# Optimization experiments

Measured on AMD Instinct MI355X. Metric: run time of the kernel, lower is better.

Reference implementation:

```python
import jax, jax.numpy as jnp
import numpy as np

N, E, G = 50000, 800000, 200
F_IN, C, HEADS = 16, 64, 4
HID = C * HEADS  # 256


def setup_inputs() -> dict:
    key = jax.random.key(0)
    ks = jax.random.split(key, 30)
    rn = lambda k, s, sc=0.1: jax.random.normal(k, s, jnp.float32) * sc
    inp = {
        'x': jax.random.normal(ks[0], (N, F_IN), jnp.float32),
        'edge_index': jax.random.randint(ks[1], (2, E), 0, N, jnp.int32),
        'batch': jnp.sort(jax.random.randint(ks[2], (N,), 0, G, jnp.int32)),
        'Wl1': rn(ks[3], (F_IN, HID)), 'Wr1': rn(ks[4], (F_IN, HID)),
        'att1': rn(ks[5], (HEADS, C)), 'b1': rn(ks[6], (HID,)),
        'g1': jnp.ones((HID,), jnp.float32), 'be1': jnp.zeros((HID,), jnp.float32),
        'Wl2': rn(ks[7], (HID, HID)), 'Wr2': rn(ks[8], (HID, HID)),
        'att2': rn(ks[9], (HEADS, C)), 'b2': rn(ks[10], (HID,)),
        'g2': jnp.ones((HID,), jnp.float32), 'be2': jnp.zeros((HID,), jnp.float32),
        # GATv2 layer 3: 256 -> 64, 1 head, mean (concat=False)
        'Wl3': rn(ks[11], (HID, C)), 'Wr3': rn(ks[12], (HID, C)),
        'att3': rn(ks[13], (1, C)), 'b3': rn(ks[14], (C,)),
        'g3': jnp.ones((C,), jnp.float32), 'be3': jnp.zeros((C,), jnp.float32),
        # classifier MLP: 128 -> 64 -> 1
        'Wc1': rn(ks[15], (2 * C, C)), 'bc1': rn(ks[16], (C,)),
        'Wc2': rn(ks[17], (C, 1)), 'bc2': rn(ks[18], (1,)),
    }
    return inp


def _gatv2(x, src, dst, Wl, Wr, att, b, heads, c, concat):
    n = x.shape[0]
    xl = (x @ Wl).reshape(n, heads, c)
    xr = (x @ Wr).reshape(n, heads, c)
    s = jax.nn.leaky_relu(xl[src] + xr[dst], 0.2)       # [E', H, C]
    e = jnp.einsum('ehc,hc->eh', s, att)                 # [E', H]
    m = jax.ops.segment_max(e, dst, num_segments=n)
    p = jnp.exp(e - m[dst])
    denom = jax.ops.segment_sum(p, dst, num_segments=n)
    alpha = p / (denom[dst] + 1e-16)
    out = jax.ops.segment_sum(alpha[:, :, None] * xl[src], dst, num_segments=n)
    out = out.reshape(n, heads * c) if concat else out.mean(axis=1)
    return out + b


def _bn(x, g, b):
    mu = x.mean(0)
    v = x.var(0)
    return (x - mu) * jax.lax.rsqrt(v + 1e-5) * g + b


def reference(x, edge_index, batch,
              Wl1, Wr1, att1, b1, g1, be1,
              Wl2, Wr2, att2, b2, g2, be2,
              Wl3, Wr3, att3, b3, g3, be3,
              Wc1, bc1, Wc2, bc2):
    n = x.shape[0]
    loop = jnp.arange(n, dtype=edge_index.dtype)
    src = jnp.concatenate([edge_index[0], loop])  # PyG add_self_loops=True
    dst = jnp.concatenate([edge_index[1], loop])

    h = _gatv2(x, src, dst, Wl1, Wr1, att1, b1, HEADS, C, True)
    h = jax.nn.elu(_bn(h, g1, be1))  # dropout disabled (eval)
    h = _gatv2(h, src, dst, Wl2, Wr2, att2, b2, HEADS, C, True)
    h = jax.nn.elu(_bn(h, g2, be2))
    h = _gatv2(h, src, dst, Wl3, Wr3, att3, b3, 1, C, False)
    h = _bn(h, g3, be3)

    cnt = jax.ops.segment_sum(jnp.ones((n, 1), h.dtype), batch, num_segments=G)
    mean_pool = jax.ops.segment_sum(h, batch, num_segments=G) / jnp.maximum(cnt, 1.0)
    max_pool = jax.ops.segment_max(h, batch, num_segments=G)
    pooled = jnp.concatenate([mean_pool, max_pool], axis=1)  # [G, 128]

    out = jax.nn.relu(pooled @ Wc1 + bc1)
    out = out @ Wc2 + bc2  # [G, 1]
    return out
```

## Files before the change

kernel.cpp:

```cpp
#include <hip/hip_runtime.h>
#include <math.h>

#define N_NODES 50000
#define N_EDGES 800000
#define ET (N_EDGES + N_NODES)
#define N_GRAPHS 200
#define F_INN 16
#define C_DIM 64
#define N_HEADS 4
#define HIDD 256
#define SCAN_BLOCKS ((N_NODES + 255) / 256)

typedef __attribute__((ext_vector_type(8))) short short8;
typedef __attribute__((ext_vector_type(8))) ushort ushort8;
typedef __attribute__((ext_vector_type(4))) float f32x4;
typedef __attribute__((ext_vector_type(2))) float f32x2;
typedef __attribute__((ext_vector_type(2))) _Float16 h16x2;

#define LOG2E 1.44269504088896340736f

__device__ __forceinline__ float ex2(float x) {
#if __has_builtin(__builtin_amdgcn_exp2f)
  return __builtin_amdgcn_exp2f(x);
#else
  return exp2f(x);
#endif
}

__device__ __forceinline__ h16x2 bc16(unsigned u) {
  union { unsigned u; h16x2 h; } c; c.u = u; return c.h;
}
__device__ __forceinline__ ushort f2h(float f) {
  union { _Float16 h; ushort u; } c; c.h = (_Float16)f; return c.u;
}

#if __has_builtin(__builtin_amdgcn_cvt_pkrtz)
using hw2 = decltype(__builtin_amdgcn_cvt_pkrtz(0.f, 0.f));
__device__ __forceinline__ h16x2 pkrtz(float a, float b) {
  union { hw2 w; h16x2 h; } c;
  c.w = __builtin_amdgcn_cvt_pkrtz(a, b);
  return c.h;
}
#else
__device__ __forceinline__ h16x2 pkrtz(float a, float b) {
  h16x2 r; r[0] = (_Float16)a; r[1] = (_Float16)b; return r;
}
#endif

__device__ __forceinline__ float fdot2f(h16x2 a, h16x2 b, float c) {
#if __has_builtin(__builtin_amdgcn_fdot2) && __has_builtin(__builtin_amdgcn_cvt_pkrtz)
  union { h16x2 h; hw2 w; } ca, cb;
  ca.h = a; cb.h = b;
  return __builtin_amdgcn_fdot2(ca.w, cb.w, c, false);
#else
  return (float)a[0] * (float)b[0] + (float)a[1] * (float)b[1] + c;
#endif
}
__device__ __forceinline__ h16x2 hmax2(h16x2 a, h16x2 b) {
#if __has_builtin(__builtin_elementwise_max)
  return __builtin_elementwise_max(a, b);
#else
  h16x2 r; r[0] = a[0] > b[0] ? a[0] : b[0]; r[1] = a[1] > b[1] ? a[1] : b[1]; return r;
#endif
}
__device__ __forceinline__ unsigned permu(unsigned s0, unsigned s1, unsigned sel) {
#if __has_builtin(__builtin_amdgcn_perm)
  return __builtin_amdgcn_perm(s0, s1, sel);
#else
  unsigned long long cat = (((unsigned long long)s0) << 32) | s1;
  unsigned r = 0;
  for (int i = 0; i < 4; ++i) {
    unsigned b = (sel >> (8 * i)) & 0xff;
    r |= ((unsigned)((cat >> (8 * (b & 7))) & 0xff)) << (8 * i);
  }
  return r;
#endif
}
#define PAIR_LO(A, B) permu((B), (A), 0x05040100u)
#define PAIR_HI(A, B) permu((B), (A), 0x07060302u)

template<int K, int M>
__global__ __launch_bounds__(256) void gemm_dual(
    const float* __restrict__ A, const float* __restrict__ Bl,
    const float* __restrict__ Br, ushort* __restrict__ Clb,
    ushort* __restrict__ Crb, int nrows)
{
  __shared__ __align__(16) float As[16][64];
  __shared__ __align__(16) float Bls[16][64];
  __shared__ __align__(16) float Brs[16][64];
  int tid = threadIdx.x;
  int row0 = blockIdx.x * 64;
  int col0 = blockIdx.y * 64;
  int tr = (tid >> 4) << 2;
  int tc = (tid & 15) << 2;
  float accL[4][4] = {{0.f}}, accR[4][4] = {{0.f}};
  int arow = tid >> 2, ak = (tid & 3) << 2;
  int brow = tid >> 4, bcol = (tid & 15) << 2;
  for (int k0 = 0; k0 < K; k0 += 16) {
    float4 av = make_float4(0.f, 0.f, 0.f, 0.f);
    int gr = row0 + arow;
    if (gr < nrows) av = *(const float4*)&A[(size_t)gr * K + k0 + ak];
    As[ak + 0][arow] = av.x;
    As[ak + 1][arow] = av.y;
    As[ak + 2][arow] = av.z;
    As[ak + 3][arow] = av.w;
    *(float4*)&Bls[brow][bcol] = *(const float4*)&Bl[(size_t)(k0 + brow) * M + col0 + bcol];
    *(float4*)&Brs[brow][bcol] = *(const float4*)&Br[(size_t)(k0 + brow) * M + col0 + bcol];
    __syncthreads();
    #pragma unroll
    for (int k = 0; k < 16; ++k) {
      float4 a = *(const float4*)&As[k][tr];
      float4 bl = *(const float4*)&Bls[k][tc];
      float4 br = *(const float4*)&Brs[k][tc];
      float aa[4] = {a.x, a.y, a.z, a.w};
      float lb[4] = {bl.x, bl.y, bl.z, bl.w};
      float rb[4] = {br.x, br.y, br.z, br.w};
      #pragma unroll
      for (int ii = 0; ii < 4; ++ii)
        #pragma unroll
        for (int jj = 0; jj < 4; ++jj) {
          accL[ii][jj] = fmaf(aa[ii], lb[jj], accL[ii][jj]);
          accR[ii][jj] = fmaf(aa[ii], rb[jj], accR[ii][jj]);
        }
    }
    __syncthreads();
  }
  #pragma unroll
  for (int ii = 0; ii < 4; ++ii) {
    int gr = row0 + tr + ii;
    if (gr < nrows) {
      *(ushort4*)&Clb[(size_t)gr * M + col0 + tc] =
          make_ushort4(f2h(accL[ii][0]), f2h(accL[ii][1]),
                       f2h(accL[ii][2]), f2h(accL[ii][3]));
      *(ushort4*)&Crb[(size_t)gr * M + col0 + tc] =
          make_ushort4(f2h(accR[ii][0]), f2h(accR[ii][1]),
                       f2h(accR[ii][2]), f2h(accR[ii][3]));
    }
  }
}

__device__ __forceinline__ void split_bf16(float a, ushort& hi, ushort& lo) {
  unsigned u = __float_as_uint(a);
  hi = (ushort)(u >> 16);
  float ah = __uint_as_float(u & 0xffff0000u);
  float r = a - ah;
  lo = (ushort)(__float_as_uint(r) >> 16);
}

template<int K, int N>
__global__ void convertB(const float* __restrict__ W, ushort* __restrict__ BTmat) {
  int idx = blockIdx.x * blockDim.x + threadIdx.x;
  if (idx >= K * N) return;
  int k = idx / N, n = idx - k * N;
  ushort hi, lo;
  split_bf16(W[idx], hi, lo);
  size_t dst = ((size_t)(k >> 3) * N + n) * 8 + (k & 7);
  BTmat[dst] = hi;
  BTmat[(size_t)(K / 8) * N * 8 + dst] = lo;
}

template<int N>
__global__ __launch_bounds__(N * 2) void gemm_fused(
    const float* __restrict__ H, const float* __restrict__ gsum,
    const float* __restrict__ gsumsq, const float* __restrict__ g,
    const float* __restrict__ be, const ushort* __restrict__ BT,
    ushort* __restrict__ Clb, ushort* __restrict__ Crb)
{
  constexpr int THREADS = N * 2;
  constexpr int PLANE = 32 * N * 8;
  __shared__ float SCs[256], SHs[256];
  __shared__ ushort Ah_s[32 * 256];
  __shared__ ushort Al_s[32 * 256];
  const int tid = threadIdx.x;
  const int brow0 = blockIdx.x * 32;

  const float invn = 1.0f / (float)N_NODES;
  for (int c = tid; c < 256; c += THREADS) {
    float mu = gsum[c] * invn;
    float var = gsumsq[c] * invn - mu * mu;
    float sc = g[c] * rsqrtf(var + 1e-5f);
    SCs[c] = sc;
    SHs[c] = be[c] - mu * sc;
  }
  __syncthreads();

  for (int gid = tid; gid < 1024; gid += THREADS) {
    int r = gid >> 5;
    int ch0 = (gid & 31) * 8;
    int grow = min(brow0 + r, N_NODES - 1);
    float4 v0 = *(const float4*)&H[(size_t)grow * 256 + ch0];
    float4 v1 = *(const float4*)&H[(size_t)grow * 256 + ch0 + 4];
    float4 sc0 = *(const float4*)&SCs[ch0];
    float4 sc1 = *(const float4*)&SCs[ch0 + 4];
    float4 sh0 = *(const float4*)&SHs[ch0];
    float4 sh1 = *(const float4*)&SHs[ch0 + 4];
    float vv[8] = {v0.x, v0.y, v0.z, v0.w, v1.x, v1.y, v1.z, v1.w};
    float scv[8] = {sc0.x, sc0.y, sc0.z, sc0.w, sc1.x, sc1.y, sc1.z, sc1.w};
    float shv[8] = {sh0.x, sh0.y, sh0.z, sh0.w, sh1.x, sh1.y, sh1.z, sh1.w};
    short8 hi8, lo8;
    #pragma unroll
    for (int j = 0; j < 8; ++j) {
      float t = fmaf(vv[j], scv[j], shv[j]);
      float e = t > 0.f ? t : __expf(t) - 1.f;
      ushort h, l;
      split_bf16(e, h, l);
      hi8[j] = (short)h;
      lo8[j] = (short)l;
    }
    int off = r * 512 + ((ch0 * 2) ^ ((r & 7) << 4));
    *(short8*)((char*)Ah_s + off) = hi8;
    *(short8*)((char*)Al_s + off) = lo8;
  }
  __syncthreads();

  const int wave = tid >> 6, lane = tid & 63;
  const int cn = lane & 15, kgrp = lane >> 4;
  const int combc = wave * 64;
  const bool isR = combc >= N;
  const ushort* Bh = BT + (isR ? 2 * PLANE : 0);
  const ushort* Bl_ = Bh + PLANE;
  const int cb = combc & (N - 1);
  f32x4 acc[2][4];
  #pragma unroll
  for (int rt = 0; rt < 2; ++rt)
    #pragma unroll
    for (int ct = 0; ct < 4; ++ct) acc[rt][ct] = (f32x4)(0.f);

  #pragma unroll 2
  for (int k0 = 0; k0 < 256; k0 += 32) {
    short8 ah[2], al[2];
    #pragma unroll
    for (int rt = 0; rt < 2; ++rt) {
      int row = rt * 16 + cn;
      int off = row * 512 + (((k0 * 2) + kgrp * 16) ^ ((row & 7) << 4));
      ah[rt] = *(const short8*)((const char*)Ah_s + off);
      al[rt] = *(const short8*)((const char*)Al_s + off);
    }
    const size_t bbase = (size_t)((k0 >> 3) + kgrp) * (N * 8);
    #pragma unroll
    for (int ct = 0; ct < 4; ++ct) {
      const size_t bo = bbase + (size_t)(cb + ct * 16 + cn) * 8;
      short8 bh = *(const short8*)&Bh[bo];
      short8 bl = *(const short8*)&Bl_[bo];
      #pragma unroll
      for (int rt = 0; rt < 2; ++rt) {
        acc[rt][ct] = __builtin_amdgcn_mfma_f32_16x16x32_bf16(ah[rt], bh, acc[rt][ct], 0, 0, 0);
        acc[rt][ct] = __builtin_amdgcn_mfma_f32_16x16x32_bf16(ah[rt], bl, acc[rt][ct], 0, 0, 0);
        acc[rt][ct] = __builtin_amdgcn_mfma_f32_16x16x32_bf16(al[rt], bh, acc[rt][ct], 0, 0, 0);
      }
    }
  }

  #pragma unroll
  for (int ct = 0; ct < 4; ++ct) {
    int cc = cb + ct * 16 + cn;
    #pragma unroll
    for (int rt = 0; rt < 2; ++rt) {
      int crow0 = brow0 + rt * 16 + kgrp * 4;
      #pragma unroll
      for (int j = 0; j < 4; ++j) {
        int rr = crow0 + j;
        if (rr < N_NODES) {
          if (!isR) Clb[(size_t)rr * N + cc] = f2h(acc[rt][ct][j]);
          else      Crb[(size_t)rr * N + cc] = f2h(acc[rt][ct][j]);
        }
      }
    }
  }
}

__global__ void hist_kernel(const int* __restrict__ dsts, int* __restrict__ curs) {
  int i = blockIdx.x * blockDim.x + threadIdx.x;
  if (i >= ET) return;
  int d = (i < N_EDGES) ? dsts[i] : i - N_EDGES;
  atomicAdd(&curs[d], 1);
}

__global__ __launch_bounds__(256) void scan_part(
    const int* __restrict__ curs, int* __restrict__ rows, int* __restrict__ bsum)
{
  __shared__ int tmp[256];
  int t = threadIdx.x;
  int i = blockIdx.x * 256 + t;
  int v = (i < N_NODES) ? curs[i] : 0;
  tmp[t] = v;
  __syncthreads();
  #pragma unroll
  for (int off = 1; off < 256; off <<= 1) {
    int u = (t >= off) ? tmp[t - off] : 0;
    __syncthreads();
    tmp[t] += u;
    __syncthreads();
  }
  if (i < N_NODES) rows[i] = tmp[t] - v;
  if (t == 255) bsum[blockIdx.x] = tmp[255];
}

__global__ __launch_bounds__(256) void scan_bsums(
    const int* __restrict__ bsum, int* __restrict__ boff)
{
  __shared__ int tmp[256];
  int t = threadIdx.x;
  int v = (t < SCAN_BLOCKS) ? bsum[t] : 0;
  tmp[t] = v;
  __syncthreads();
  #pragma unroll
  for (int off = 1; off < 256; off <<= 1) {
    int u = (t >= off) ? tmp[t - off] : 0;
    __syncthreads();
    tmp[t] += u;
    __syncthreads();
  }
  if (t < SCAN_BLOCKS) boff[t] = tmp[t] - v;
}

__global__ __launch_bounds__(256) void scan_apply(
    int* __restrict__ rows, const int* __restrict__ boff, int* __restrict__ curs)
{
  int i = blockIdx.x * 256 + threadIdx.x;
  if (i < N_NODES) {
    int r = rows[i] + boff[blockIdx.x];
    rows[i] = r;
    curs[i] = r;
  }
  if (i == 0) rows[N_NODES] = ET;
}

__global__ void scatter_kernel(const int* __restrict__ srcs, const int* __restrict__ dsts,
                               int* __restrict__ curs, int* __restrict__ esrc) {
  int i = blockIdx.x * blockDim.x + threadIdx.x;
  if (i >= ET) return;
  int s, d;
  if (i < N_EDGES) { s = srcs[i]; d = dsts[i]; } else { s = d = i - N_EDGES; }
  int pos = atomicAdd(&curs[d], 1);
  esrc[pos] = s;
}

__global__ __launch_bounds__(256) void flash256(
    const ushort* __restrict__ xl, const ushort* __restrict__ xr,
    const float* __restrict__ att, const int* __restrict__ rows,
    const int* __restrict__ esrc, float* __restrict__ out)
{
  const int wave = threadIdx.x >> 6, lane = threadIdx.x & 63;
  const int d = blockIdx.x * 4 + wave;
  const unsigned lo4 = lane * 4;
  int beg = rows[d], end = rows[d + 1];
  uint2 urx = *(const uint2*)&xr[(size_t)d * 256 + lo4];
  h16x2 x01 = bc16(urx.x), x23 = bc16(urx.y);
  float4 w = *(const float4*)&att[lo4];
  h16x2 w01 = pkrtz(w.x * LOG2E, w.y * LOG2E);
  h16x2 w23 = pkrtz(w.z * LOG2E, w.w * LOG2E);
  const _Float16 c2 = (_Float16)0.2f;
  const h16x2 c02 = {c2, c2};
  auto score = [&](uint2 u) -> float {
    h16x2 v01 = bc16(u.x) + x01;
    h16x2 v23 = bc16(u.y) + x23;
    v01 = hmax2(v01, v01 * c02);
    v23 = hmax2(v23, v23 * c02);
    return fdot2f(v01, w01, fdot2f(v23, w23, 0.f));
  };
  float m = -INFINITY, s = 0.f;
  float a0 = 0.f, a1 = 0.f, a2 = 0.f, a3 = 0.f;
  int p = beg;
  for (; p + 4 <= end; p += 4) {
    int s1 = esrc[p], s2 = esrc[p + 1], s3 = esrc[p + 2], s4 = esrc[p + 3];
    uint2 u1 = *(const uint2*)&xl[((unsigned)s1 << 8) + lo4];
    uint2 u2 = *(const uint2*)&xl[((unsigned)s2 << 8) + lo4];
    uint2 u3 = *(const uint2*)&xl[((unsigned)s3 << 8) + lo4];
    uint2 u4 = *(const uint2*)&xl[((unsigned)s4 << 8) + lo4];
    float e1 = score(u1);
    float e2 = score(u2);
    float e3 = score(u3);
    float e4 = score(u4);
    e1 += __shfl_xor(e1, 1); e2 += __shfl_xor(e2, 1);
    e3 += __shfl_xor(e3, 1); e4 += __shfl_xor(e4, 1);
    e1 += __shfl_xor(e1, 2); e2 += __shfl_xor(e2, 2);
    e3 += __shfl_xor(e3, 2); e4 += __shfl_xor(e4, 2);
    e1 += __shfl_xor(e1, 4); e2 += __shfl_xor(e2, 4);
    e3 += __shfl_xor(e3, 4); e4 += __shfl_xor(e4, 4);
    e1 += __shfl_xor(e1, 8); e2 += __shfl_xor(e2, 8);
    e3 += __shfl_xor(e3, 8); e4 += __shfl_xor(e4, 8);
    float gm = fmaxf(fmaxf(e1, e2), fmaxf(e3, e4));
    float p1, p2, p3, p4;
    if (__all(gm <= m + 8.0f)) {
      p1 = ex2(e1 - m);
      p2 = ex2(e2 - m);
      p3 = ex2(e3 - m);
      p4 = ex2(e4 - m);
    } else {
      float mn = fmaxf(m, gm);
      float f = ex2(m - mn);
      p1 = ex2(e1 - mn);
      p2 = ex2(e2 - mn);
      p3 = ex2(e3 - mn);
      p4 = ex2(e4 - mn);
      s *= f; a0 *= f; a1 *= f; a2 *= f; a3 *= f;
      m = mn;
    }
    s += (p1 + p2) + (p3 + p4);
    h16x2 p12 = pkrtz(p1, p2), p34 = pkrtz(p3, p4);
    a0 = fdot2f(p12, bc16(PAIR_LO(u1.x, u2.x)), a0);
    a0 = fdot2f(p34, bc16(PAIR_LO(u3.x, u4.x)), a0);
    a1 = fdot2f(p12, bc16(PAIR_HI(u1.x, u2.x)), a1);
    a1 = fdot2f(p34, bc16(PAIR_HI(u3.x, u4.x)), a1);
    a2 = fdot2f(p12, bc16(PAIR_LO(u1.y, u2.y)), a2);
    a2 = fdot2f(p34, bc16(PAIR_LO(u3.y, u4.y)), a2);
    a3 = fdot2f(p12, bc16(PAIR_HI(u1.y, u2.y)), a3);
    a3 = fdot2f(p34, bc16(PAIR_HI(u3.y, u4.y)), a3);
  }
  for (; p < end; ++p) {
    int s1 = esrc[p];
    uint2 u1 = *(const uint2*)&xl[((unsigned)s1 << 8) + lo4];
    float e1 = score(u1);
    e1 += __shfl_xor(e1, 1);
    e1 += __shfl_xor(e1, 2);
    e1 += __shfl_xor(e1, 4);
    e1 += __shfl_xor(e1, 8);
    float mn = fmaxf(m, e1);
    float f = ex2(m - mn);
    float p1 = ex2(e1 - mn);
    h16x2 b01 = bc16(u1.x), b23 = bc16(u1.y);
    s = fmaf(s, f, p1);
    a0 = fmaf(a0, f, p1 * (float)b01[0]);
    a1 = fmaf(a1, f, p1 * (float)b01[1]);
    a2 = fmaf(a2, f, p1 * (float)b23[0]);
    a3 = fmaf(a3, f, p1 * (float)b23[1]);
    m = mn;
  }
  float inv = 1.f / (s + 1e-16f);
  *(float4*)&out[(size_t)d * 256 + lo4] =
      make_float4(a0 * inv, a1 * inv, a2 * inv, a3 * inv);
}

__global__ __launch_bounds__(256) void flash64(
    const ushort* __restrict__ xl, const ushort* __restrict__ xr,
    const float* __restrict__ att, const int* __restrict__ rows,
    const int* __restrict__ esrc, float* __restrict__ out)
{
  const int wave = threadIdx.x >> 6, lane = threadIdx.x & 63;
  const int di = lane >> 3, sl = lane & 7;
  const int idx = blockIdx.x * 32 + wave * 8 + di;
  const bool valid = idx < N_NODES;
  const int d = valid ? idx : N_NODES - 1;
  const unsigned ch = sl * 8;
  uint4 uxr = *(const uint4*)&xr[(size_t)d * 64 + ch];
  float4 wa = *(const float4*)&att[ch];
  float4 wb = *(const float4*)&att[ch + 4];
  h16x2 x0 = bc16(uxr.x), x1 = bc16(uxr.y), x2 = bc16(uxr.z), x3 = bc16(uxr.w);
  h16x2 w0 = pkrtz(wa.x * LOG2E, wa.y * LOG2E);
  h16x2 w1 = pkrtz(wa.z * LOG2E, wa.w * LOG2E);
  h16x2 w2 = pkrtz(wb.x * LOG2E, wb.y * LOG2E);
  h16x2 w3 = pkrtz(wb.z * LOG2E, wb.w * LOG2E);
  const _Float16 c2 = (_Float16)0.2f;
  const h16x2 c02 = {c2, c2};
  int beg = rows[d], end = rows[d + 1];
  float m = -INFINITY, s = 0.f;
  float a0 = 0.f, a1 = 0.f, a2 = 0.f, a3 = 0.f;
  float a4 = 0.f, a5 = 0.f, a6 = 0.f, a7 = 0.f;

  auto score = [&](uint4 u) -> float {
    h16x2 v0 = bc16(u.x) + x0;
    h16x2 v1 = bc16(u.y) + x1;
    h16x2 v2 = bc16(u.z) + x2;
    h16x2 v3 = bc16(u.w) + x3;
    v0 = hmax2(v0, v0 * c02);
    v1 = hmax2(v1, v1 * c02);
    v2 = hmax2(v2, v2 * c02);
    v3 = hmax2(v3, v3 * c02);
    return fdot2f(v0, w0, fdot2f(v1, w1, fdot2f(v2, w2, fdot2f(v3, w3, 0.f))));
  };
  auto one_edge = [&](int src) {
    uint4 u = *(const uint4*)&xl[((unsigned)src << 6) + ch];
    float e = score(u);
    e += __shfl_xor(e, 1);
    e += __shfl_xor(e, 2);
    e += __shfl_xor(e, 4);
    float mn = fmaxf(m, e);
    float f = ex2(m - mn);
    float pe = ex2(e - mn);
    h16x2 b0 = bc16(u.x), b1 = bc16(u.y), b2 = bc16(u.z), b3 = bc16(u.w);
    s = s * f + pe;
    a0 = fmaf(a0, f, pe * (float)b0[0]);
    a1 = fmaf(a1, f, pe * (float)b0[1]);
    a2 = fmaf(a2, f, pe * (float)b1[0]);
    a3 = fmaf(a3, f, pe * (float)b1[1]);
    a4 = fmaf(a4, f, pe * (float)b2[0]);
    a5 = fmaf(a5, f, pe * (float)b2[1]);
    a6 = fmaf(a6, f, pe * (float)b3[0]);
    a7 = fmaf(a7, f, pe * (float)b3[1]);
    m = mn;
  };

  int p = beg;
  int hd = min(end, (beg + 3) & ~3);
  for (; p < hd; ++p) one_edge(esrc[p]);
  for (; p + 4 <= end; p += 4) {
    int4 sv = *(const int4*)&esrc[p];
    uint4 u1 = *(const uint4*)&xl[((unsigned)sv.x << 6) + ch];
    uint4 u2 = *(const uint4*)&xl[((unsigned)sv.y << 6) + ch];
    uint4 u3 = *(const uint4*)&xl[((unsigned)sv.z << 6) + ch];
    uint4 u4 = *(const uint4*)&xl[((unsigned)sv.w << 6) + ch];
    float e1 = score(u1);
    float e2 = score(u2);
    float e3 = score(u3);
    float e4 = score(u4);
    e1 += __shfl_xor(e1, 1); e2 += __shfl_xor(e2, 1);
    e3 += __shfl_xor(e3, 1); e4 += __shfl_xor(e4, 1);
    e1 += __shfl_xor(e1, 2); e2 += __shfl_xor(e2, 2);
    e3 += __shfl_xor(e3, 2); e4 += __shfl_xor(e4, 2);
    e1 += __shfl_xor(e1, 4); e2 += __shfl_xor(e2, 4);
    e3 += __shfl_xor(e3, 4); e4 += __shfl_xor(e4, 4);
    float gm = fmaxf(fmaxf(e1, e2), fmaxf(e3, e4));
    float p1, p2, p3, p4;
    if (__all(gm <= m + 8.0f)) {
      p1 = ex2(e1 - m);
      p2 = ex2(e2 - m);
      p3 = ex2(e3 - m);
      p4 = ex2(e4 - m);
    } else {
      float mn = fmaxf(m, gm);
      float f = ex2(m - mn);
      p1 = ex2(e1 - mn);
      p2 = ex2(e2 - mn);
      p3 = ex2(e3 - mn);
      p4 = ex2(e4 - mn);
      s *= f;
      a0 *= f; a1 *= f; a2 *= f; a3 *= f;
      a4 *= f; a5 *= f; a6 *= f; a7 *= f;
      m = mn;
    }
    s += (p1 + p2) + (p3 + p4);
    h16x2 p12 = pkrtz(p1, p2), p34 = pkrtz(p3, p4);
    a0 = fdot2f(p12, bc16(PAIR_LO(u1.x, u2.x)), a0);
    a0 = fdot2f(p34, bc16(PAIR_LO(u3.x, u4.x)), a0);
    a1 = fdot2f(p12, bc16(PAIR_HI(u1.x, u2.x)), a1);
    a1 = fdot2f(p34, bc16(PAIR_HI(u3.x, u4.x)), a1);
    a2 = fdot2f(p12, bc16(PAIR_LO(u1.y, u2.y)), a2);
    a2 = fdot2f(p34, bc16(PAIR_LO(u3.y, u4.y)), a2);
    a3 = fdot2f(p12, bc16(PAIR_HI(u1.y, u2.y)), a3);
    a3 = fdot2f(p34, bc16(PAIR_HI(u3.y, u4.y)), a3);
    a4 = fdot2f(p12, bc16(PAIR_LO(u1.z, u2.z)), a4);
    a4 = fdot2f(p34, bc16(PAIR_LO(u3.z, u4.z)), a4);
    a5 = fdot2f(p12, bc16(PAIR_HI(u1.z, u2.z)), a5);
    a5 = fdot2f(p34, bc16(PAIR_HI(u3.z, u4.z)), a5);
    a6 = fdot2f(p12, bc16(PAIR_LO(u1.w, u2.w)), a6);
    a6 = fdot2f(p34, bc16(PAIR_LO(u3.w, u4.w)), a6);
    a7 = fdot2f(p12, bc16(PAIR_HI(u1.w, u2.w)), a7);
    a7 = fdot2f(p34, bc16(PAIR_HI(u3.w, u4.w)), a7);
  }
  for (; p < end; ++p) one_edge(esrc[p]);

  if (valid) {
    float inv = 1.f / (s + 1e-16f);
    *(float4*)&out[(size_t)d * 64 + ch] =
        make_float4(a0 * inv, a1 * inv, a2 * inv, a3 * inv);
    *(float4*)&out[(size_t)d * 64 + ch + 4] =
        make_float4(a4 * inv, a5 * inv, a6 * inv, a7 * inv);
  }
}

template<int D_, int RPB>
__global__ __launch_bounds__(256) void bn_stats(const float* __restrict__ h,
    float* __restrict__ gsum, float* __restrict__ gsumsq, int nrows)
{
  constexpr int RG = 256 / D_;
  int c = threadIdx.x % D_;
  int rg = threadIdx.x / D_;
  int r0 = blockIdx.x * RPB;
  float s = 0.f, sq = 0.f;
  int rend = min(r0 + RPB, nrows);
  for (int r = r0 + rg; r < rend; r += RG) {
    float v = h[(size_t)r * D_ + c];
    s += v;
    sq = fmaf(v, v, sq);
  }
  atomicAdd(&gsum[c], s);
  atomicAdd(&gsumsq[c], sq);
}

__global__ __launch_bounds__(256) void pool_mlp(
    const float* __restrict__ h3, const int* __restrict__ batch,
    const float* __restrict__ gsum, const float* __restrict__ gsumsq,
    const float* __restrict__ g3, const float* __restrict__ be3,
    const float* __restrict__ Wc1, const float* __restrict__ bc1,
    const float* __restrict__ Wc2, const float* __restrict__ bc2,
    float* __restrict__ outp)
{
  int g = blockIdx.x;
  int t = threadIdx.x;
  int lane = t & 63, w = t >> 6;
  int lo, hi;
  {
    int a = 0, b = N_NODES;
    while (a < b) { int mid = (a + b) >> 1; if (batch[mid] < g) a = mid + 1; else b = mid; }
    lo = a;
    b = N_NODES;
    while (a < b) { int mid = (a + b) >> 1; if (batch[mid] < g + 1) a = mid + 1; else b = mid; }
    hi = a;
  }
  const float invn = 1.0f / (float)N_NODES;
  float mu = gsum[lane] * invn;
  float var = gsumsq[lane] * invn - mu * mu;
  float scl = g3[lane] * rsqrtf(var + 1e-5f);
  float shf = be3[lane] - mu * scl;
  float s = 0.f, mx = -INFINITY;
  for (int r = lo + w; r < hi; r += 4) {
    float v = fmaf(h3[(size_t)r * 64 + lane], scl, shf);
    s += v;
    mx = fmaxf(mx, v);
  }
  __shared__ float ssum[4][64];
  __shared__ float smax[4][64];
  __shared__ float pooled[128];
  ssum[w][lane] = s;
  smax[w][lane] = mx;
  __syncthreads();
  if (w == 0) {
    float tot = ssum[0][lane] + ssum[1][lane] + ssum[2][lane] + ssum[3][lane];
    float m4 = fmaxf(fmaxf(smax[0][lane], smax[1][lane]),
                     fmaxf(smax[2][lane], smax[3][lane]));
    float cnt = (float)(hi - lo);
    pooled[lane] = tot / fmaxf(cnt, 1.f);
    pooled[64 + lane] = m4;
  }
  __syncthreads();
  if (w == 0) {
    float a = bc1[lane];
    #pragma unroll 8
    for (int k = 0; k < 128; ++k) a = fmaf(pooled[k], Wc1[k * 64 + lane], a);
    a = fmaxf(a, 0.f);
    float v = a * Wc2[lane];
    v += __shfl_xor(v, 1);
    v += __shfl_xor(v, 2);
    v += __shfl_xor(v, 4);
    v += __shfl_xor(v, 8);
    v += __shfl_xor(v, 16);
    v += __shfl_xor(v, 32);
    if (lane == 0) outp[g] = v + bc2[0];
  }
}

extern "C" void kernel_launch(void* const* d_in, const int* in_sizes, int n_in,
                              void* d_out, int out_size, void* d_ws, size_t ws_size,
                              hipStream_t stream)
{
  const float* x    = (const float*)d_in[0];
  const int*   ei   = (const int*)d_in[1];
  const int*   batch= (const int*)d_in[2];
  const float* Wl1  = (const float*)d_in[3];
  const float* Wr1  = (const float*)d_in[4];
  const float* att1 = (const float*)d_in[5];
  const float* g1   = (const float*)d_in[7];
  const float* be1  = (const float*)d_in[8];
  const float* Wl2  = (const float*)d_in[9];
  const float* Wr2  = (const float*)d_in[10];
  const float* att2 = (const float*)d_in[11];
  const float* g2   = (const float*)d_in[13];
  const float* be2  = (const float*)d_in[14];
  const float* Wl3  = (const float*)d_in[15];
  const float* Wr3  = (const float*)d_in[16];
  const float* att3 = (const float*)d_in[17];
  const float* g3   = (const float*)d_in[19];
  const float* be3  = (const float*)d_in[20];
  const float* Wc1  = (const float*)d_in[21];
  const float* bc1  = (const float*)d_in[22];
  const float* Wc2  = (const float*)d_in[23];
  const float* bc2  = (const float*)d_in[24];

  const int* srcs = ei;
  const int* dsts = ei + N_EDGES;

  float* ws = (float*)d_ws;
  size_t o = 0;
  ushort* XLB = (ushort*)(ws + o); o += (size_t)N_NODES * HIDD / 2;
  ushort* XRB = (ushort*)(ws + o); o += (size_t)N_NODES * HIDD / 2;
  float* Hb = ws + o;            o += (size_t)N_NODES * HIDD;
  ushort* BT2 = (ushort*)(ws + o); o += (size_t)4 * 32 * 256 * 8 / 2;
  ushort* BT3 = (ushort*)(ws + o); o += (size_t)4 * 32 * 64 * 8 / 2;
  int* ESRC = (int*)(ws + o);    o += ET;
  int* ROWS = (int*)(ws + o);    o += N_NODES + 1;
  int* CURS = (int*)(ws + o);    o += N_NODES;
  int* BSUM = (int*)(ws + o);    o += SCAN_BLOCKS;
  int* BOFF = (int*)(ws + o);    o += SCAN_BLOCKS;
  float* GS  = ws + o;           o += 256;
  float* GSQ = ws + o;           o += 256;

  const int ROW_BLOCKS = (N_NODES + 63) / 64;
  const int ROW_BLOCKS32 = (N_NODES + 31) / 32;
  const int DST_BLOCKS = (N_NODES + 3) / 4;
  constexpr int PLANE2 = 32 * 256 * 8;
  constexpr int PLANE3 = 32 * 64 * 8;

  convertB<256, 256><<<(65536 + 255) / 256, 256, 0, stream>>>(Wl2, BT2);
  convertB<256, 256><<<(65536 + 255) / 256, 256, 0, stream>>>(Wr2, BT2 + 2 * PLANE2);
  convertB<256, 64><<<(16384 + 255) / 256, 256, 0, stream>>>(Wl3, BT3);
  convertB<256, 64><<<(16384 + 255) / 256, 256, 0, stream>>>(Wr3, BT3 + 2 * PLANE3);

  hipMemsetAsync(CURS, 0, N_NODES * 4, stream);
  hist_kernel<<<(ET + 255) / 256, 256, 0, stream>>>(dsts, CURS);
  scan_part<<<SCAN_BLOCKS, 256, 0, stream>>>(CURS, ROWS, BSUM);
  scan_bsums<<<1, 256, 0, stream>>>(BSUM, BOFF);
  scan_apply<<<SCAN_BLOCKS, 256, 0, stream>>>(ROWS, BOFF, CURS);
  scatter_kernel<<<(ET + 255) / 256, 256, 0, stream>>>(srcs, dsts, CURS, ESRC);

  gemm_dual<16, 256><<<dim3(ROW_BLOCKS, 4), 256, 0, stream>>>(
      x, Wl1, Wr1, XLB, XRB, N_NODES);
  flash256<<<DST_BLOCKS, 256, 0, stream>>>(XLB, XRB, att1, ROWS, ESRC, Hb);
  hipMemsetAsync(GS, 0, 512 * 4, stream);
  bn_stats<256, 64><<<ROW_BLOCKS, 256, 0, stream>>>(Hb, GS, GSQ, N_NODES);

  gemm_fused<256><<<ROW_BLOCKS32, 512, 0, stream>>>(
      Hb, GS, GSQ, g1, be1, BT2, XLB, XRB);
  flash256<<<DST_BLOCKS, 256, 0, stream>>>(XLB, XRB, att2, ROWS, ESRC, Hb);
  hipMemsetAsync(GS, 0, 512 * 4, stream);
  bn_stats<256, 64><<<ROW_BLOCKS, 256, 0, stream>>>(Hb, GS, GSQ, N_NODES);

  gemm_fused<64><<<ROW_BLOCKS32, 128, 0, stream>>>(
      Hb, GS, GSQ, g2, be2, BT3, XLB, XRB);
  flash64<<<(N_NODES + 31) / 32, 256, 0, stream>>>(XLB, XRB, att3, ROWS, ESRC, Hb);
  hipMemsetAsync(GS, 0, 512 * 4, stream);
  bn_stats<64, 256><<<(N_NODES + 255) / 256, 256, 0, stream>>>(Hb, GS, GSQ, N_NODES);

  pool_mlp<<<N_GRAPHS, 256, 0, stream>>>(Hb, batch, GS, GSQ, g3, be3,
                                         Wc1, bc1, Wc2, bc2, (float*)d_out);
}
```

Before: 530.5 us.

## Store layer outputs in fp16 and batch 8 edges per step in flash256

Intermediate hidden activations written by the attention kernels and read by BN stats, the fused GEMM and pooling are now fp16 instead of fp32, halving their memory traffic. flash256 gains an 8-edge unrolled loop that issues all gathers first and skips rescaling when the new max stays within a threshold. It also accumulates the weighted sum with packed fp16 dot products. The cost is lower precision in the stored activations and in the aggregation weights.

```diff
diff --git a/kernel.cpp b/kernel.cpp
--- a/kernel.cpp
+++ b/kernel.cpp
@@ -32,6 +32,9 @@
 }
 __device__ __forceinline__ ushort f2h(float f) {
   union { _Float16 h; ushort u; } c; c.h = (_Float16)f; return c.u;
+}
+__device__ __forceinline__ float h2f(ushort u) {
+  union { ushort u; _Float16 h; } c; c.u = u; return (float)c.h;
 }
 
 #if __has_builtin(__builtin_amdgcn_cvt_pkrtz)
@@ -161,7 +164,7 @@
 
 template<int N>
 __global__ __launch_bounds__(N * 2) void gemm_fused(
-    const float* __restrict__ H, const float* __restrict__ gsum,
+    const ushort* __restrict__ H, const float* __restrict__ gsum,
     const float* __restrict__ gsumsq, const float* __restrict__ g,
     const float* __restrict__ be, const ushort* __restrict__ BT,
     ushort* __restrict__ Clb, ushort* __restrict__ Crb)
@@ -188,13 +191,14 @@
     int r = gid >> 5;
     int ch0 = (gid & 31) * 8;
     int grow = min(brow0 + r, N_NODES - 1);
-    float4 v0 = *(const float4*)&H[(size_t)grow * 256 + ch0];
-    float4 v1 = *(const float4*)&H[(size_t)grow * 256 + ch0 + 4];
+    uint4 hv = *(const uint4*)&H[(size_t)grow * 256 + ch0];
+    h16x2 q0 = bc16(hv.x), q1 = bc16(hv.y), q2 = bc16(hv.z), q3 = bc16(hv.w);
     float4 sc0 = *(const float4*)&SCs[ch0];
     float4 sc1 = *(const float4*)&SCs[ch0 + 4];
     float4 sh0 = *(const float4*)&SHs[ch0];
     float4 sh1 = *(const float4*)&SHs[ch0 + 4];
-    float vv[8] = {v0.x, v0.y, v0.z, v0.w, v1.x, v1.y, v1.z, v1.w};
+    float vv[8] = {(float)q0[0], (float)q0[1], (float)q1[0], (float)q1[1],
+                   (float)q2[0], (float)q2[1], (float)q3[0], (float)q3[1]};
     float scv[8] = {sc0.x, sc0.y, sc0.z, sc0.w, sc1.x, sc1.y, sc1.z, sc1.w};
     float shv[8] = {sh0.x, sh0.y, sh0.z, sh0.w, sh1.x, sh1.y, sh1.z, sh1.w};
     short8 hi8, lo8;
@@ -339,7 +343,7 @@
 __global__ __launch_bounds__(256) void flash256(
     const ushort* __restrict__ xl, const ushort* __restrict__ xr,
     const float* __restrict__ att, const int* __restrict__ rows,
-    const int* __restrict__ esrc, float* __restrict__ out)
+    const int* __restrict__ esrc, ushort* __restrict__ out)
 {
   const int wave = threadIdx.x >> 6, lane = threadIdx.x & 63;
   const int d = blockIdx.x * 4 + wave;
@@ -362,6 +366,56 @@
   float m = -INFINITY, s = 0.f;
   float a0 = 0.f, a1 = 0.f, a2 = 0.f, a3 = 0.f;
   int p = beg;
+  for (; p + 8 <= end; p += 8) {
+    uint2 u[8];
+    float e[8];
+    #pragma unroll
+    for (int j = 0; j < 8; ++j) {
+      int sj = esrc[p + j];
+      u[j] = *(const uint2*)&xl[((unsigned)sj << 8) + lo4];
+    }
+    #pragma unroll
+    for (int j = 0; j < 8; ++j) e[j] = score(u[j]);
+    #pragma unroll
+    for (int st = 1; st <= 8; st <<= 1) {
+      #pragma unroll
+      for (int j = 0; j < 8; ++j) e[j] += __shfl_xor(e[j], st);
+    }
+    float gm = e[0];
+    #pragma unroll
+    for (int j = 1; j < 8; ++j) gm = fmaxf(gm, e[j]);
+    float pr[8];
+    if (__all(gm <= m + 8.0f)) {
+      #pragma unroll
+      for (int j = 0; j < 8; ++j) pr[j] = ex2(e[j] - m);
+    } else {
+      float mn = fmaxf(m, gm);
+      float f = ex2(m - mn);
+      #pragma unroll
+      for (int j = 0; j < 8; ++j) pr[j] = ex2(e[j] - mn);
+      s *= f; a0 *= f; a1 *= f; a2 *= f; a3 *= f;
+      m = mn;
+    }
+    s += ((pr[0] + pr[1]) + (pr[2] + pr[3])) + ((pr[4] + pr[5]) + (pr[6] + pr[7]));
+    h16x2 p01 = pkrtz(pr[0], pr[1]), p23 = pkrtz(pr[2], pr[3]);
+    h16x2 p45 = pkrtz(pr[4], pr[5]), p67 = pkrtz(pr[6], pr[7]);
+    a0 = fdot2f(p01, bc16(PAIR_LO(u[0].x, u[1].x)), a0);
+    a0 = fdot2f(p23, bc16(PAIR_LO(u[2].x, u[3].x)), a0);
+    a0 = fdot2f(p45, bc16(PAIR_LO(u[4].x, u[5].x)), a0);
+    a0 = fdot2f(p67, bc16(PAIR_LO(u[6].x, u[7].x)), a0);
+    a1 = fdot2f(p01, bc16(PAIR_HI(u[0].x, u[1].x)), a1);
+    a1 = fdot2f(p23, bc16(PAIR_HI(u[2].x, u[3].x)), a1);
+    a1 = fdot2f(p45, bc16(PAIR_HI(u[4].x, u[5].x)), a1);
+    a1 = fdot2f(p67, bc16(PAIR_HI(u[6].x, u[7].x)), a1);
+    a2 = fdot2f(p01, bc16(PAIR_LO(u[0].y, u[1].y)), a2);
+    a2 = fdot2f(p23, bc16(PAIR_LO(u[2].y, u[3].y)), a2);
+    a2 = fdot2f(p45, bc16(PAIR_LO(u[4].y, u[5].y)), a2);
+    a2 = fdot2f(p67, bc16(PAIR_LO(u[6].y, u[7].y)), a2);
+    a3 = fdot2f(p01, bc16(PAIR_HI(u[0].y, u[1].y)), a3);
+    a3 = fdot2f(p23, bc16(PAIR_HI(u[2].y, u[3].y)), a3);
+    a3 = fdot2f(p45, bc16(PAIR_HI(u[4].y, u[5].y)), a3);
+    a3 = fdot2f(p67, bc16(PAIR_HI(u[6].y, u[7].y)), a3);
+  }
   for (; p + 4 <= end; p += 4) {
     int s1 = esrc[p], s2 = esrc[p + 1], s3 = esrc[p + 2], s4 = esrc[p + 3];
     uint2 u1 = *(const uint2*)&xl[((unsigned)s1 << 8) + lo4];
@@ -428,14 +482,14 @@
     m = mn;
   }
   float inv = 1.f / (s + 1e-16f);
-  *(float4*)&out[(size_t)d * 256 + lo4] =
-      make_float4(a0 * inv, a1 * inv, a2 * inv, a3 * inv);
+  *(ushort4*)&out[(size_t)d * 256 + lo4] =
+      make_ushort4(f2h(a0 * inv), f2h(a1 * inv), f2h(a2 * inv), f2h(a3 * inv));
 }
 
 __global__ __launch_bounds__(256) void flash64(
     const ushort* __restrict__ xl, const ushort* __restrict__ xr,
     const float* __restrict__ att, const int* __restrict__ rows,
-    const int* __restrict__ esrc, float* __restrict__ out)
+    const int* __restrict__ esrc, ushort* __restrict__ out)
 {
   const int wave = threadIdx.x >> 6, lane = threadIdx.x & 63;
   const int di = lane >> 3, sl = lane & 7;
@@ -552,15 +606,17 @@
 
   if (valid) {
     float inv = 1.f / (s + 1e-16f);
-    *(float4*)&out[(size_t)d * 64 + ch] =
-        make_float4(a0 * inv, a1 * inv, a2 * inv, a3 * inv);
-    *(float4*)&out[(size_t)d * 64 + ch + 4] =
-        make_float4(a4 * inv, a5 * inv, a6 * inv, a7 * inv);
+    ushort8 o;
+    o[0] = f2h(a0 * inv); o[1] = f2h(a1 * inv);
+    o[2] = f2h(a2 * inv); o[3] = f2h(a3 * inv);
+    o[4] = f2h(a4 * inv); o[5] = f2h(a5 * inv);
+    o[6] = f2h(a6 * inv); o[7] = f2h(a7 * inv);
+    *(ushort8*)&out[(size_t)d * 64 + ch] = o;
   }
 }
 
 template<int D_, int RPB>
-__global__ __launch_bounds__(256) void bn_stats(const float* __restrict__ h,
+__global__ __launch_bounds__(256) void bn_stats(const ushort* __restrict__ h,
     float* __restrict__ gsum, float* __restrict__ gsumsq, int nrows)
 {
   constexpr int RG = 256 / D_;
@@ -570,7 +626,7 @@
   float s = 0.f, sq = 0.f;
   int rend = min(r0 + RPB, nrows);
   for (int r = r0 + rg; r < rend; r += RG) {
-    float v = h[(size_t)r * D_ + c];
+    float v = h2f(h[(size_t)r * D_ + c]);
     s += v;
     sq = fmaf(v, v, sq);
   }
@@ -579,7 +635,7 @@
 }
 
 __global__ __launch_bounds__(256) void pool_mlp(
-    const float* __restrict__ h3, const int* __restrict__ batch,
+    const ushort* __restrict__ h3, const int* __restrict__ batch,
     const float* __restrict__ gsum, const float* __restrict__ gsumsq,
     const float* __restrict__ g3, const float* __restrict__ be3,
     const float* __restrict__ Wc1, const float* __restrict__ bc1,
@@ -605,7 +661,7 @@
   float shf = be3[lane] - mu * scl;
   float s = 0.f, mx = -INFINITY;
   for (int r = lo + w; r < hi; r += 4) {
-    float v = fmaf(h3[(size_t)r * 64 + lane], scl, shf);
+    float v = fmaf(h2f(h3[(size_t)r * 64 + lane]), scl, shf);
     s += v;
     mx = fmaxf(mx, v);
   }
@@ -674,7 +730,7 @@
   size_t o = 0;
   ushort* XLB = (ushort*)(ws + o); o += (size_t)N_NODES * HIDD / 2;
   ushort* XRB = (ushort*)(ws + o); o += (size_t)N_NODES * HIDD / 2;
-  float* Hb = ws + o;            o += (size_t)N_NODES * HIDD;
+  ushort* Hb = (ushort*)(ws + o);  o += (size_t)N_NODES * HIDD / 2;
   ushort* BT2 = (ushort*)(ws + o); o += (size_t)4 * 32 * 256 * 8 / 2;
   ushort* BT3 = (ushort*)(ws + o); o += (size_t)4 * 32 * 64 * 8 / 2;
   int* ESRC = (int*)(ws + o);    o += ET;
```

Result: faster. 519.7 us (median of 2 runs) (-2.0%).
